# Kernel optimization log

Hardware: AMD Instinct MI355X
Metric: run time of the kernel (lower is better)

The kernel has to match this reference:

```python
import jax, jax.numpy as jnp
import numpy as np

B, T, D, H, HS = 2, 256, 2048, 32, 64
LORA, DLORA, ST = 32, 64, 66  # maa lora rank, decay lora rank, state rows (2+HS)
EPS = 1e-5


def setup_inputs() -> dict:
    key = jax.random.key(0)
    ks = jax.random.split(key, 24)
    n = lambda k, sh, s=0.02: (jax.random.normal(k, sh, jnp.float32) * s)
    u = lambda k, sh: jax.random.uniform(k, sh, jnp.float32)
    return {
        "x": jax.random.normal(ks[0], (B, T, D), jnp.float32),
        "state": jax.random.normal(ks[1], (B, ST, D), jnp.float32) * 0.1,
        "ln1_w": jnp.ones((D,), jnp.float32),
        "ln1_b": jnp.zeros((D,), jnp.float32),
        "time_maa_x": u(ks[2], (D,)),
        "time_maa_w1": n(ks[3], (D, 5 * LORA)),
        "time_maa_w2": n(ks[4], (5, LORA, D)),
        "time_maa_k": u(ks[5], (D,)),
        "time_maa_w": u(ks[6], (D,)),
        "time_maa_v": u(ks[7], (D,)),
        "time_maa_r": u(ks[8], (D,)),
        "time_maa_g": u(ks[9], (D,)),
        "time_decay": n(ks[10], (D,), 0.5),
        "time_decay_w1": n(ks[11], (D, DLORA)),
        "time_decay_w2": n(ks[12], (DLORA, D)),
        "time_faaaa": n(ks[13], (H, HS, 1), 0.1),
        "receptance_weight": n(ks[14], (D, D)),
        "key_weight": n(ks[15], (D, D)),
        "value_weight": n(ks[16], (D, D)),
        "output_weight": n(ks[17], (D, D)),
        "gate_weight": n(ks[18], (D, D)),
        "lnx_w": jnp.ones((D,), jnp.float32),
        "lnx_b": jnp.zeros((D,), jnp.float32),
        "i": 0,
    }


def reference(x, state, ln1_w, ln1_b, time_maa_x, time_maa_w1, time_maa_w2,
              time_maa_k, time_maa_w, time_maa_v, time_maa_r, time_maa_g,
              time_decay, time_decay_w1, time_decay_w2, time_faaaa,
              receptance_weight, key_weight, value_weight, output_weight,
              gate_weight, lnx_w, lnx_b, i):
    # forward() early-returns time_mixing(ln1(x), state, i)
    mu = x.mean(-1, keepdims=True)
    var = ((x - mu) ** 2).mean(-1, keepdims=True)
    x = (x - mu) * jax.lax.rsqrt(var + EPS) * ln1_w + ln1_b

    i1 = (2 + HS) * i + 1
    # token shift: sx[t] = x[t-1] - x[t], with state row i1 as x[-1]
    sx = jnp.concatenate([state[:, i1][:, None] - x[:, :1], x[:, :-1] - x[:, 1:]], axis=1)

    xxx = x + sx * time_maa_x
    t5 = jnp.tanh(xxx @ time_maa_w1).reshape(B, T, 5, LORA)
    xxx5 = jnp.einsum('btfr,frd->btfd', t5, time_maa_w2)          # [B,T,5,D]
    maa = jnp.stack([time_maa_k, time_maa_w, time_maa_v, time_maa_r, time_maa_g])  # [5,D]
    x5 = x[:, :, None] + sx[:, :, None] * (maa + xxx5)            # [B,T,5,D]

    k = (x5[:, :, 0] @ key_weight.T).reshape(B, T, H, HS)
    w = jnp.exp(-jnp.exp(time_decay + jnp.tanh(x5[:, :, 1] @ time_decay_w1) @ time_decay_w2)).reshape(B, T, H, HS)
    v = (x5[:, :, 2] @ value_weight.T).reshape(B, T, H, HS)
    r = (x5[:, :, 3] @ receptance_weight.T).reshape(B, T, H, HS)
    g = jax.nn.silu(x5[:, :, 4] @ gate_weight.T)                  # [B,T,D]

    kv = jnp.einsum('bthi,bthj->bthij', k, v)                     # [B,T,H,HS,HS]
    prev0 = state[:, i1 + 1:i1 + 1 + HS].reshape(B, H, HS, HS)

    def step(prev, xs):
        kv_t, w_t = xs
        return kv_t + w_t[..., None] * prev, prev  # emit state BEFORE update

    _, state_s = jax.lax.scan(step, prev0,
                              (kv.transpose(1, 0, 2, 3, 4), w.transpose(1, 0, 2, 3)))
    state_s = state_s.transpose(1, 0, 2, 3, 4)                    # [B,T,H,HS,HS]

    wkv = time_faaaa * kv + state_s
    rwkv = jnp.einsum('bthj,bthjd->bthd', r, wkv)                 # [B,T,H,HS]

    # GroupNorm(num_groups=H) over each head's HS channels
    gm = rwkv.mean(-1, keepdims=True)
    gv = ((rwkv - gm) ** 2).mean(-1, keepdims=True)
    normed = (rwkv - gm) * jax.lax.rsqrt(gv + EPS)
    normed = normed * lnx_w.reshape(H, HS) + lnx_b.reshape(H, HS)
    normed = normed.reshape(B, T, D)

    return (normed * g) @ output_weight.T
```

## Files before the change

### kernel.cpp

```cpp
#include <hip/hip_runtime.h>
#include <hip/hip_bf16.h>

typedef unsigned short u16;
typedef __attribute__((ext_vector_type(4))) float f32x4;
typedef __attribute__((ext_vector_type(8))) short short8;
typedef __attribute__((ext_vector_type(4))) short bf16x4;

#define B_ 2
#define T_ 256
#define D_ 2048
#define H_ 32
#define HS_ 64
#define M_ 512
#define ST_ 66
#define EPS_ 1e-5f
#define NC_ 16
#define CL_ 16

__device__ __forceinline__ float bf2f(u16 u) {
    union { unsigned int i; float f; } c; c.i = ((unsigned int)u) << 16; return c.f;
}
__device__ __forceinline__ u16 f2bf(float f) {
    union { unsigned int i; float f; } c; c.f = f;
    unsigned int r = c.i + 0x7fffu + ((c.i >> 16) & 1u);
    return (u16)(r >> 16);
}

__device__ __forceinline__ void gld16(const u16* g, u16* l) {
    __builtin_amdgcn_global_load_lds((const __attribute__((address_space(1))) void*)g,
                                     (__attribute__((address_space(3))) void*)l, 16, 0, 0);
}

__global__ __launch_bounds__(256) void wcvt_kernel(const float* __restrict__ wk, const float* __restrict__ wv,
                                                   const float* __restrict__ wr, const float* __restrict__ wg,
                                                   const float* __restrict__ wo, u16* __restrict__ out)
{
    const int wsel = blockIdx.y;
    const float* in = (wsel == 0) ? wk : (wsel == 1) ? wv : (wsel == 2) ? wr : (wsel == 3) ? wg : wo;
    const size_t e = ((size_t)blockIdx.x * 256 + threadIdx.x) * 8;
    f32x4 a = *(const f32x4*)(in + e);
    f32x4 b = *(const f32x4*)(in + e + 4);
    short8 o;
#pragma unroll
    for (int i = 0; i < 4; i++) { o[i] = (short)f2bf(a[i]); o[i + 4] = (short)f2bf(b[i]); }
    *(short8*)(out + (size_t)wsel * D_ * D_ + e) = o;
}

__global__ __launch_bounds__(256) void ln_kernel(const float* __restrict__ x, const float* __restrict__ w,
                                                 const float* __restrict__ bias, float* __restrict__ xln)
{
    const int row = blockIdx.x;
    const float* xr = x + (size_t)row * D_;
    float* orow = xln + (size_t)row * D_;
    const int t = threadIdx.x;
    f32x4 a0 = *(const f32x4*)(xr + t * 8);
    f32x4 a1 = *(const f32x4*)(xr + t * 8 + 4);
    float s = 0.f, q = 0.f;
#pragma unroll
    for (int i = 0; i < 4; i++) { s += a0[i] + a1[i]; q += a0[i]*a0[i] + a1[i]*a1[i]; }
#pragma unroll
    for (int off = 1; off < 64; off <<= 1) { s += __shfl_xor(s, off, 64); q += __shfl_xor(q, off, 64); }
    __shared__ float ls[4], lq[4];
    const int wid = t >> 6, lane = t & 63;
    if (lane == 0) { ls[wid] = s; lq[wid] = q; }
    __syncthreads();
    s = ls[0] + ls[1] + ls[2] + ls[3];
    q = lq[0] + lq[1] + lq[2] + lq[3];
    const float mu = s * (1.f / D_);
    const float var = q * (1.f / D_) - mu * mu;
    const float rs = rsqrtf(var + EPS_);
#pragma unroll
    for (int i = 0; i < 8; i++) {
        int d = t * 8 + i;
        float f = (i < 4) ? a0[i] : a1[i - 4];
        orow[d] = (f - mu) * rs * w[d] + bias[d];
    }
}

__global__ __launch_bounds__(256) void shift_kernel(const float* __restrict__ xln, const float* __restrict__ state,
                                                    const float* __restrict__ maax, const int* __restrict__ ip,
                                                    float* __restrict__ sx, u16* __restrict__ xxxb)
{
    const size_t gid = (size_t)blockIdx.x * 256 + threadIdx.x;
    const size_t e = gid * 4;
    const int row = (int)(e >> 11);
    const int d = (int)(e & 2047);
    const int tt = row & (T_ - 1);
    const int b = row >> 8;
    const float* prev;
    if (tt == 0) prev = state + ((size_t)b * ST_ + (size_t)(66 * ip[0] + 1)) * D_ + d;
    else         prev = xln + e - D_;
    f32x4 p = *(const f32x4*)prev;
    f32x4 c = *(const f32x4*)(xln + e);
    f32x4 mx = *(const f32x4*)(maax + d);
    f32x4 sv;
    bf16x4 xv;
#pragma unroll
    for (int i = 0; i < 4; i++) { sv[i] = p[i] - c[i]; xv[i] = (short)f2bf(c[i] + sv[i] * mx[i]); }
    *(f32x4*)(sx + e) = sv;
    *(bf16x4*)(xxxb + e) = xv;
}

__global__ __launch_bounds__(256) void txp_kernel(const float* __restrict__ in, u16* __restrict__ out,
                                                  int K, int N)
{
    __shared__ float tile[32][33];
    const int k0 = blockIdx.x * 32, n0 = blockIdx.y * 32;
    const int c = threadIdx.x & 31, r8 = threadIdx.x >> 5;
#pragma unroll
    for (int i = 0; i < 4; i++) {
        int r = r8 + i * 8;
        tile[r][c] = in[(size_t)(k0 + r) * N + (n0 + c)];
    }
    __syncthreads();
#pragma unroll
    for (int i = 0; i < 4; i++) {
        int r = r8 + i * 8;
        out[(size_t)(n0 + r) * K + (k0 + c)] = f2bf(tile[c][r]);
    }
}

template<bool TANH>
__global__ __launch_bounds__(512) void wdot_kernel(const u16* __restrict__ A, const u16* __restrict__ Wt,
                                                   float* __restrict__ C, int N)
{
    const int gw = (int)((blockIdx.x * 512 + threadIdx.x) >> 6);
    const int lane = threadIdx.x & 63;
    const int m = gw / N, n = gw - m * N;
    const u16* a = A + (size_t)m * D_ + lane * 8;
    const u16* w = Wt + (size_t)n * D_ + lane * 8;
    float acc = 0.f;
#pragma unroll
    for (int i = 0; i < 4; i++) {
        short8 av = *(const short8*)(a + i * 512);
        short8 wv = *(const short8*)(w + i * 512);
#pragma unroll
        for (int j = 0; j < 8; j++)
            acc = fmaf(bf2f((u16)av[j]), bf2f((u16)wv[j]), acc);
    }
#pragma unroll
    for (int off = 1; off < 64; off <<= 1) acc += __shfl_xor(acc, off, 64);
    if (lane == 0) C[gw] = TANH ? tanhf(acc) : acc;
}

__global__ __launch_bounds__(256) void maa2_kernel(const float* __restrict__ t5, const float* __restrict__ w2,
                                                   const float* __restrict__ xln, const float* __restrict__ sxp,
                                                   const float* __restrict__ mk, const float* __restrict__ mw,
                                                   const float* __restrict__ mv, const float* __restrict__ mr,
                                                   const float* __restrict__ mg, u16* __restrict__ x5)
{
    const int gid = blockIdx.x * 256 + threadIdx.x;
    const int d = gid & (D_ - 1);
    const int f = (gid >> 11) % 5;
    const int mg4 = gid / (5 * D_);
    const float* maa = (f == 0) ? mk : (f == 1) ? mw : (f == 2) ? mv : (f == 3) ? mr : mg;
    const float mf = maa[d];
    const float* w2f = w2 + (size_t)f * 32 * D_ + d;
    const float* t5b = t5 + (size_t)mg4 * 4 * 160 + f * 32;
    float a0 = 0, a1 = 0, a2 = 0, a3 = 0;
#pragma unroll 8
    for (int r = 0; r < 32; r++) {
        float wv = w2f[(size_t)r * D_];
        a0 = fmaf(t5b[r], wv, a0);
        a1 = fmaf(t5b[160 + r], wv, a1);
        a2 = fmaf(t5b[320 + r], wv, a2);
        a3 = fmaf(t5b[480 + r], wv, a3);
    }
    const float accs[4] = {a0, a1, a2, a3};
    const size_t m0 = (size_t)mg4 * 4;
#pragma unroll
    for (int mm = 0; mm < 4; mm++) {
        size_t e = (m0 + mm) * D_ + d;
        x5[(size_t)f * M_ * D_ + e] = f2bf(xln[e] + sxp[e] * (mf + accs[mm]));
    }
}

__global__ __launch_bounds__(256) void decay2_kernel(const float* __restrict__ td, const float* __restrict__ dw2,
                                                     const float* __restrict__ tdec, float* __restrict__ wout)
{
    const int gid = blockIdx.x * 256 + threadIdx.x;
    const int d = gid & (D_ - 1);
    const int mg4 = gid >> 11;
    const float* wp = dw2 + d;
    const float* tb = td + (size_t)mg4 * 4 * 64;
    float a0 = 0, a1 = 0, a2 = 0, a3 = 0;
#pragma unroll 8
    for (int r = 0; r < 64; r++) {
        float wv = wp[(size_t)r * D_];
        a0 = fmaf(tb[r], wv, a0);
        a1 = fmaf(tb[64 + r], wv, a1);
        a2 = fmaf(tb[128 + r], wv, a2);
        a3 = fmaf(tb[192 + r], wv, a3);
    }
    const float base = tdec[d];
    const float accs[4] = {a0, a1, a2, a3};
#pragma unroll
    for (int mm = 0; mm < 4; mm++)
        wout[((size_t)mg4 * 4 + mm) * D_ + d] = expf(-expf(base + accs[mm]));
}

__device__ __forceinline__ void gemm2p_body(const u16* __restrict__ A, const u16* __restrict__ Wb,
                                            float* __restrict__ C, int m0, int n0, int k0, int KC)
{
    __shared__ u16 As[2][128 * 64];
    __shared__ u16 Bs[2][64 * 64];
    const int tid = threadIdx.x;
    const int lane = tid & 63;
    const int wvd = tid >> 6;
    const int wm = (wvd >> 1) * 64;
    const int wn = (wvd & 1) * 32;

    f32x4 acc[4][2];
#pragma unroll
    for (int i = 0; i < 4; i++)
#pragma unroll
        for (int j = 0; j < 2; j++) { acc[i][j][0]=0.f; acc[i][j][1]=0.f; acc[i][j][2]=0.f; acc[i][j][3]=0.f; }

    const int srow = tid >> 3;
    const int sw8  = (((tid & 7) ^ (srow & 7)) << 3);
    const u16* Ag = A + (size_t)(m0 + srow) * D_ + k0 + sw8;
    const u16* Wg = Wb + (size_t)(n0 + srow) * D_ + k0 + sw8;
    const int ldst = tid * 8;

    const int rsw = (lane & 7) << 3;
    const int colb = (lane >> 4) * 8;
    const int fr = lane & 15;

#define STAGE_(bb, kt)                                                            \
    {                                                                             \
        _Pragma("unroll")                                                         \
        for (int i = 0; i < 4; i++)                                               \
            gld16(Ag + (size_t)(i * 32) * D_ + (kt), &As[bb][i * 2048 + ldst]);   \
        _Pragma("unroll")                                                         \
        for (int i = 0; i < 2; i++)                                               \
            gld16(Wg + (size_t)(i * 32) * D_ + (kt), &Bs[bb][i * 2048 + ldst]);   \
    }

    STAGE_(0, 0);
    __syncthreads();
    int cur = 0;
    for (int kt = 0; kt < KC; kt += 64) {
        if (kt + 64 < KC) STAGE_(cur ^ 1, kt + 64);
#pragma unroll
        for (int kk = 0; kk < 64; kk += 32) {
            const int c = (kk + colb) ^ rsw;
            short8 av[4], bv[2];
#pragma unroll
            for (int mi = 0; mi < 4; mi++)
                av[mi] = *(const short8*)&As[cur][(wm + mi * 16 + fr) * 64 + c];
#pragma unroll
            for (int ni = 0; ni < 2; ni++)
                bv[ni] = *(const short8*)&Bs[cur][(wn + ni * 16 + fr) * 64 + c];
#pragma unroll
            for (int mi = 0; mi < 4; mi++)
#pragma unroll
                for (int ni = 0; ni < 2; ni++)
                    acc[mi][ni] = __builtin_amdgcn_mfma_f32_16x16x32_bf16(av[mi], bv[ni], acc[mi][ni], 0, 0, 0);
        }
        __syncthreads();
        cur ^= 1;
    }
#undef STAGE_
    const int cr = wm + (lane >> 4) * 4;
    const int cc = wn + fr;
#pragma unroll
    for (int mi = 0; mi < 4; mi++)
#pragma unroll
        for (int ni = 0; ni < 2; ni++)
#pragma unroll
            for (int j = 0; j < 4; j++)
                C[(size_t)(m0 + cr + mi * 16 + j) * D_ + (n0 + cc + ni * 16)] = acc[mi][ni][j];
}

__global__ __launch_bounds__(256) void gemm4g_kernel(const u16* __restrict__ x5, const u16* __restrict__ wcvt,
                                                     float* __restrict__ kvK, float* __restrict__ kvV,
                                                     float* __restrict__ kvR, float* __restrict__ kvG)
{
    const int s = blockIdx.z;
    const u16* A = x5 + (size_t)(s == 0 ? 0 : s + 1) * M_ * D_;
    const u16* W = wcvt + (size_t)s * D_ * D_;
    float* C = (s == 0) ? kvK : (s == 1) ? kvV : (s == 2) ? kvR : kvG;
    gemm2p_body(A, W, C, blockIdx.y * 128, blockIdx.x * 64, 0, D_);
}

__global__ __launch_bounds__(256) void gemm1g_kernel(const u16* __restrict__ y, const u16* __restrict__ wo,
                                                     float* __restrict__ out, float* __restrict__ p0,
                                                     float* __restrict__ p1, float* __restrict__ p2)
{
    const int ks = blockIdx.z;
    float* C = (ks == 0) ? out : (ks == 1) ? p0 : (ks == 2) ? p1 : p2;
    gemm2p_body(y, wo, C, blockIdx.y * 128, blockIdx.x * 64, ks * 512, 512);
}

__global__ __launch_bounds__(256) void add3_kernel(float* __restrict__ dst, const float* __restrict__ s0,
                                                   const float* __restrict__ s1, const float* __restrict__ s2)
{
    const size_t e = ((size_t)blockIdx.x * 256 + threadIdx.x) * 4;
    f32x4 d = *(const f32x4*)(dst + e);
    f32x4 a = *(const f32x4*)(s0 + e);
    f32x4 b = *(const f32x4*)(s1 + e);
    f32x4 c = *(const f32x4*)(s2 + e);
#pragma unroll
    for (int i = 0; i < 4; i++) d[i] += (a[i] + b[i]) + c[i];
    *(f32x4*)(dst + e) = d;
}

__global__ __launch_bounds__(512) void rec1_kernel(const float* __restrict__ rB, const float* __restrict__ kB,
                                                   const float* __restrict__ wB, const float* __restrict__ vB,
                                                   const float* __restrict__ fa, float* __restrict__ rwkv,
                                                   float* __restrict__ CS, float* __restrict__ RP,
                                                   float* __restrict__ PC)
{
    const int bx = blockIdx.x;
    const int c  = bx & (NC_ - 1);
    const int bh = bx >> 4;
    const int h = bh & 31, b = bh >> 5;
    const int tid = threadIdx.x;
    const int wv = tid >> 6, lane = tid & 63;
    const int wg = wv >> 2;
    const int jb = lane >> 3, dsub = lane & 7;
    const int jbase = jb * 8;
    const int d0 = wg * 32 + (wv & 3) * 8 + dsub;

    __shared__ float stage[4][CL_][64];
    __shared__ float p2[CL_][8][64];
    __shared__ float p1[CL_][8];
    __shared__ float rpS[CL_ * 64];

    float S[8], pv[8], faj[8];
#pragma unroll
    for (int q = 0; q < 8; q++) { S[q] = 0.f; pv[q] = 1.f; faj[q] = fa[h * 64 + jbase + q]; }

    const size_t base = ((size_t)b * T_ * H_ + h) * HS_;
    const int t0 = c * CL_;
    const int arr = wv & 3;
    const float* mysrc = (arr == 0) ? rB : (arr == 1) ? kB : (arr == 2) ? wB : vB;
    const int ts0 = wg * 8 + (lane >> 4);
    const int sch = (lane & 15) * 4;
    const bool p1w = (wv == 0 && dsub == 0);

#pragma unroll
    for (int p = 0; p < 2; p++) {
        f32x4 v = *(const f32x4*)(mysrc + base + (size_t)(t0 + ts0 + p * 4) * (H_ * HS_) + sch);
        *(f32x4*)&stage[arr][ts0 + p * 4][sch] = v;
    }
    __syncthreads();

    f32x4 r0 = *(const f32x4*)&stage[0][0][jbase];
    f32x4 r1 = *(const f32x4*)&stage[0][0][jbase + 4];
    f32x4 k0 = *(const f32x4*)&stage[1][0][jbase];
    f32x4 k1 = *(const f32x4*)&stage[1][0][jbase + 4];
    f32x4 w0 = *(const f32x4*)&stage[2][0][jbase];
    f32x4 w1 = *(const f32x4*)&stage[2][0][jbase + 4];
    float vd = stage[3][0][d0];
#pragma unroll
    for (int ts = 0; ts < CL_; ++ts) {
        f32x4 nr0 = r0, nr1 = r1, nk0 = k0, nk1 = k1, nw0 = w0, nw1 = w1;
        float nvd = vd;
        if (ts + 1 < CL_) {
            nr0 = *(const f32x4*)&stage[0][ts + 1][jbase];
            nr1 = *(const f32x4*)&stage[0][ts + 1][jbase + 4];
            nk0 = *(const f32x4*)&stage[1][ts + 1][jbase];
            nk1 = *(const f32x4*)&stage[1][ts + 1][jbase + 4];
            nw0 = *(const f32x4*)&stage[2][ts + 1][jbase];
            nw1 = *(const f32x4*)&stage[2][ts + 1][jbase + 4];
            nvd = stage[3][ts + 1][d0];
        }
        float s1 = 0.f, s2 = 0.f;
#pragma unroll
        for (int q = 0; q < 4; q++) {
            s1 = fmaf(r0[q] * faj[q],     k0[q], s1);
            s1 = fmaf(r1[q] * faj[q + 4], k1[q], s1);
            s2 = fmaf(r0[q], S[q],     s2);
            s2 = fmaf(r1[q], S[q + 4], s2);
        }
        p2[ts][jb][d0 ^ (jb << 3)] = s2;
        if (p1w) {
            p1[ts][jb] = s1;
#pragma unroll
            for (int q = 0; q < 4; q++) {
                rpS[ts * 64 + jbase + q]     = r0[q] * pv[q];
                rpS[ts * 64 + jbase + 4 + q] = r1[q] * pv[q + 4];
            }
        }
#pragma unroll
        for (int q = 0; q < 4; q++) {
            pv[q]     *= w0[q];
            pv[q + 4] *= w1[q];
            S[q]       = fmaf(w0[q], S[q],     k0[q] * vd);
            S[q + 4]   = fmaf(w1[q], S[q + 4], k1[q] * vd);
        }
        r0 = nr0; r1 = nr1; k0 = nk0; k1 = nk1; w0 = nw0; w1 = nw1; vd = nvd;
    }
    __syncthreads();
#pragma unroll
    for (int p = 0; p < 2; p++) {
        const int ts = wv * 2 + p;
        f32x4 p1a = *(const f32x4*)&p1[ts][0];
        f32x4 p1b = *(const f32x4*)&p1[ts][4];
        float s1t = ((p1a[0] + p1a[1]) + (p1a[2] + p1a[3])) +
                    ((p1b[0] + p1b[1]) + (p1b[2] + p1b[3]));
        float s2t = 0.f;
#pragma unroll
        for (int j = 0; j < 8; j++) s2t += p2[ts][j][lane ^ (j << 3)];
        const float vvv = stage[3][ts][lane];
        rwkv[base + (size_t)(t0 + ts) * (H_ * HS_) + lane] = fmaf(vvv, s1t, s2t);
    }
    RP[(size_t)bx * (CL_ * 64) + tid]       = rpS[tid];
    RP[(size_t)bx * (CL_ * 64) + 512 + tid] = rpS[512 + tid];
#pragma unroll
    for (int q = 0; q < 8; q++)
        CS[(size_t)bx * 4096 + (size_t)(jbase + q) * 64 + d0] = S[q];
    if (p1w) {
#pragma unroll
        for (int q = 0; q < 8; q++)
            PC[(size_t)bx * 64 + jbase + q] = pv[q];
    }
}

__global__ __launch_bounds__(512) void rec2_kernel(const float* __restrict__ state, const int* __restrict__ ip,
                                                   float* __restrict__ CS, const float* __restrict__ PC)
{
    const int bh = blockIdx.x;
    const int b = bh >> 5, h = bh & 31;
    const int tid = threadIdx.x;
    const int o = tid * 8;
    const int jrow = tid >> 3;
    const float* Sp = state + (size_t)b * ST_ * D_ + (size_t)(66 * ip[0] + 2) * D_ + (size_t)h * HS_ * HS_;
    f32x4 c0 = *(const f32x4*)(Sp + o);
    f32x4 c1 = *(const f32x4*)(Sp + o + 4);
    for (int c = 0; c < NC_; ++c) {
        float* cs = CS + ((size_t)(bh * NC_ + c)) * 4096 + o;
        f32x4 l0 = *(const f32x4*)cs;
        f32x4 l1 = *(const f32x4*)(cs + 4);
        const float pc = PC[(size_t)(bh * NC_ + c) * 64 + jrow];
        f32x4 n0, n1;
#pragma unroll
        for (int i = 0; i < 4; i++) { n0[i] = fmaf(pc, c0[i], l0[i]); n1[i] = fmaf(pc, c1[i], l1[i]); }
        *(f32x4*)cs = c0;
        *(f32x4*)(cs + 4) = c1;
        c0 = n0; c1 = n1;
    }
}

__global__ __launch_bounds__(256) void rec3_kernel(const float* __restrict__ CS, const float* __restrict__ RP,
                                                   float* __restrict__ rwkv)
{
    const int bx = blockIdx.x;
    const int c  = bx & (NC_ - 1);
    const int bh = bx >> 4;
    const int h = bh & 31, b = bh >> 5;
    const int tid = threadIdx.x;
    __shared__ float Ss[4096];
    __shared__ float rp[CL_ * 64];
#pragma unroll
    for (int i = 0; i < 4; i++)
        *(f32x4*)&Ss[tid * 4 + i * 1024] = *(const f32x4*)(CS + (size_t)bx * 4096 + tid * 4 + i * 1024);
    *(f32x4*)&rp[tid * 4] = *(const f32x4*)(RP + (size_t)bx * (CL_ * 64) + tid * 4);
    __syncthreads();
    const int tl = tid >> 4;
    const int d4 = (tid & 15) * 4;
    f32x4 acc; acc[0] = acc[1] = acc[2] = acc[3] = 0.f;
    const float* rpr = &rp[tl * 64];
#pragma unroll 16
    for (int j = 0; j < 64; ++j) {
        const float rv = rpr[j];
        const f32x4 sv = *(const f32x4*)&Ss[j * 64 + d4];
#pragma unroll
        for (int i = 0; i < 4; i++) acc[i] = fmaf(rv, sv[i], acc[i]);
    }
    const size_t base = ((size_t)b * T_ * H_ + h) * HS_;
    float* o = rwkv + base + (size_t)(c * CL_ + tl) * (H_ * HS_) + d4;
    f32x4 cur = *(const f32x4*)o;
#pragma unroll
    for (int i = 0; i < 4; i++) cur[i] += acc[i];
    *(f32x4*)o = cur;
}

__global__ __launch_bounds__(256) void gn_kernel(const float* __restrict__ rwkv, const float* __restrict__ gpre,
                                                 const float* __restrict__ lnxw, const float* __restrict__ lnxb,
                                                 u16* __restrict__ y)
{
    const int g = blockIdx.x * 4 + (threadIdx.x >> 6);
    const int lane = threadIdx.x & 63;
    const size_t e = (size_t)g * 64 + lane;
    const float val = rwkv[e];
    float s = val, q = val * val;
#pragma unroll
    for (int off = 1; off < 64; off <<= 1) { s += __shfl_xor(s, off, 64); q += __shfl_xor(q, off, 64); }
    const float mu = s * (1.f / 64.f);
    const float var = q * (1.f / 64.f) - mu * mu;
    const float rs = rsqrtf(var + EPS_);
    const int hj = (int)(e & (size_t)(D_ - 1));
    const float nrm = (val - mu) * rs * lnxw[hj] + lnxb[hj];
    const float gp = gpre[e];
    const float gv = gp / (1.f + expf(-gp));
    y[e] = f2bf(nrm * gv);
}

extern "C" void kernel_launch(void* const* d_in, const int* in_sizes, int n_in,
                              void* d_out, int out_size, void* d_ws, size_t ws_size,
                              hipStream_t stream)
{
    const float* x     = (const float*)d_in[0];
    const float* state = (const float*)d_in[1];
    const float* ln1w  = (const float*)d_in[2];
    const float* ln1b  = (const float*)d_in[3];
    const float* maax  = (const float*)d_in[4];
    const float* w1    = (const float*)d_in[5];
    const float* w2    = (const float*)d_in[6];
    const float* maak  = (const float*)d_in[7];
    const float* maaw  = (const float*)d_in[8];
    const float* maav  = (const float*)d_in[9];
    const float* maar  = (const float*)d_in[10];
    const float* maag  = (const float*)d_in[11];
    const float* tdec  = (const float*)d_in[12];
    const float* dw1   = (const float*)d_in[13];
    const float* dw2   = (const float*)d_in[14];
    const float* fa    = (const float*)d_in[15];
    const float* wrec  = (const float*)d_in[16];
    const float* wkey  = (const float*)d_in[17];
    const float* wval  = (const float*)d_in[18];
    const float* wout  = (const float*)d_in[19];
    const float* wgate = (const float*)d_in[20];
    const float* lnxw  = (const float*)d_in[21];
    const float* lnxb  = (const float*)d_in[22];
    const int*   ip    = (const int*)d_in[23];

    char* ws = (char*)d_ws;
    const size_t MD = (size_t)M_ * D_;
    u16*   wcvt = (u16*)  (ws);
    float* xln  = (float*)(ws + ((size_t)40 << 20));
    float* sx   = (float*)(ws + ((size_t)44 << 20));
    u16*   xxxb = (u16*)  (ws + ((size_t)48 << 20));
    u16*   w1t  = (u16*)  (ws + ((size_t)50 << 20));
    u16*   dw1t = (u16*)  (ws + ((size_t)51 << 20));
    float* t5   = (float*)(ws + ((size_t)52 << 20));
    float* td   = (float*)(ws + ((size_t)53 << 20));
    u16*   x5   = (u16*)  (ws + ((size_t)54 << 20));
    float* wdec = (float*)(ws + ((size_t)64 << 20));
    float* kvK  = (float*)(ws + ((size_t)40 << 20));
    float* kvV  = (float*)(ws + ((size_t)44 << 20));
    float* kvR  = (float*)(ws + ((size_t)48 << 20));
    float* kvG  = (float*)(ws + ((size_t)68 << 20));
    float* rwkv = (float*)(ws + ((size_t)72 << 20));
    u16*   y    = (u16*)  (ws + ((size_t)76 << 20));
    float* CS   = (float*)(ws);
    float* RP   = (float*)(ws + ((size_t)16 << 20));
    float* PC   = (float*)(ws + ((size_t)20 << 20));
    float* pp0  = (float*)(ws + ((size_t)54 << 20));
    float* pp1  = (float*)(ws + ((size_t)58 << 20));
    float* pp2  = (float*)(ws + ((size_t)62 << 20));
    float* out  = (float*)d_out;

    hipLaunchKernelGGL(wcvt_kernel,   dim3(2048, 5),  dim3(256), 0, stream, wkey, wval, wrec, wgate, wout, wcvt);
    hipLaunchKernelGGL(ln_kernel,     dim3(512),      dim3(256), 0, stream, x, ln1w, ln1b, xln);
    hipLaunchKernelGGL(shift_kernel,  dim3(1024),     dim3(256), 0, stream, xln, state, maax, ip, sx, xxxb);
    hipLaunchKernelGGL(txp_kernel,    dim3(64, 5),    dim3(256), 0, stream, w1, w1t, D_, 160);
    hipLaunchKernelGGL(txp_kernel,    dim3(64, 2),    dim3(256), 0, stream, dw1, dw1t, D_, 64);
    hipLaunchKernelGGL((wdot_kernel<true>), dim3(10240), dim3(512), 0, stream, xxxb, w1t, t5, 160);
    hipLaunchKernelGGL(maa2_kernel,   dim3(5120),     dim3(256), 0, stream, t5, w2, xln, sx, maak, maaw, maav, maar, maag, x5);
    hipLaunchKernelGGL((wdot_kernel<true>), dim3(4096), dim3(512), 0, stream, x5 + MD, dw1t, td, 64);
    hipLaunchKernelGGL(decay2_kernel, dim3(1024),     dim3(256), 0, stream, td, dw2, tdec, wdec);
    hipLaunchKernelGGL(gemm4g_kernel, dim3(32, 4, 4), dim3(256), 0, stream, x5, wcvt, kvK, kvV, kvR, kvG);
    hipLaunchKernelGGL(rec1_kernel,   dim3(B_ * H_ * NC_), dim3(512), 0, stream, kvR, kvK, wdec, kvV, fa, rwkv, CS, RP, PC);
    hipLaunchKernelGGL(rec2_kernel,   dim3(B_ * H_),  dim3(512), 0, stream, state, ip, CS, PC);
    hipLaunchKernelGGL(rec3_kernel,   dim3(B_ * H_ * NC_), dim3(256), 0, stream, CS, RP, rwkv);
    hipLaunchKernelGGL(gn_kernel,     dim3(4096),     dim3(256), 0, stream, rwkv, kvG, lnxw, lnxb, y);
    hipLaunchKernelGGL(gemm1g_kernel, dim3(32, 4, 4), dim3(256), 0, stream, y, wcvt + (size_t)4 * D_ * D_, out, pp0, pp1, pp2);
    hipLaunchKernelGGL(add3_kernel,   dim3(1024),     dim3(256), 0, stream, out, pp0, pp1, pp2);

    (void)in_sizes; (void)n_in; (void)out_size; (void)ws_size;
}
```

Baseline: 197.4 us.

## Fuse weight bf16 conversion into GEMM loads, merge rec3 with groupnorm, restructure maa2

Removes the separate weight-conversion pass. The GEMMs now read fp32 weights straight from global memory, convert them to bf16 in registers and write them into swizzled LDS. This removes a full read and write of five 2048x2048 matrices, but doubles the bytes each GEMM block loads for B and drops async global_load_lds for that operand. The rec3 and groupnorm kernels are fused so rwkv is not written and read back. maa2 now handles all five mixes per thread, reusing the xln and sx loads across them.

```diff
diff --git a/kernel.cpp b/kernel.cpp
--- a/kernel.cpp
+++ b/kernel.cpp
@@ -25,25 +25,14 @@
     unsigned int r = c.i + 0x7fffu + ((c.i >> 16) & 1u);
     return (u16)(r >> 16);
 }
+__device__ __forceinline__ u16 f2bf_hw(float f) {
+    __hip_bfloat16 b = __float2bfloat16(f);
+    return *reinterpret_cast<u16*>(&b);
+}
 
 __device__ __forceinline__ void gld16(const u16* g, u16* l) {
     __builtin_amdgcn_global_load_lds((const __attribute__((address_space(1))) void*)g,
                                      (__attribute__((address_space(3))) void*)l, 16, 0, 0);
-}
-
-__global__ __launch_bounds__(256) void wcvt_kernel(const float* __restrict__ wk, const float* __restrict__ wv,
-                                                   const float* __restrict__ wr, const float* __restrict__ wg,
-                                                   const float* __restrict__ wo, u16* __restrict__ out)
-{
-    const int wsel = blockIdx.y;
-    const float* in = (wsel == 0) ? wk : (wsel == 1) ? wv : (wsel == 2) ? wr : (wsel == 3) ? wg : wo;
-    const size_t e = ((size_t)blockIdx.x * 256 + threadIdx.x) * 8;
-    f32x4 a = *(const f32x4*)(in + e);
-    f32x4 b = *(const f32x4*)(in + e + 4);
-    short8 o;
-#pragma unroll
-    for (int i = 0; i < 4; i++) { o[i] = (short)f2bf(a[i]); o[i + 4] = (short)f2bf(b[i]); }
-    *(short8*)(out + (size_t)wsel * D_ * D_ + e) = o;
 }
 
 __global__ __launch_bounds__(256) void ln_kernel(const float* __restrict__ x, const float* __restrict__ w,
@@ -151,27 +140,36 @@
 {
     const int gid = blockIdx.x * 256 + threadIdx.x;
     const int d = gid & (D_ - 1);
-    const int f = (gid >> 11) % 5;
-    const int mg4 = gid / (5 * D_);
-    const float* maa = (f == 0) ? mk : (f == 1) ? mw : (f == 2) ? mv : (f == 3) ? mr : mg;
-    const float mf = maa[d];
-    const float* w2f = w2 + (size_t)f * 32 * D_ + d;
-    const float* t5b = t5 + (size_t)mg4 * 4 * 160 + f * 32;
-    float a0 = 0, a1 = 0, a2 = 0, a3 = 0;
+    const int mg4 = gid >> 11;
+    const size_t m0 = (size_t)mg4 * 4;
+    float xl[4], sv[4];
+#pragma unroll
+    for (int mm = 0; mm < 4; mm++) {
+        const size_t e = (m0 + mm) * D_ + d;
+        xl[mm] = xln[e];
+        sv[mm] = sxp[e];
+    }
+    const float* t5b = t5 + m0 * 160;
+#pragma unroll
+    for (int f = 0; f < 5; f++) {
+        const float* maa = (f == 0) ? mk : (f == 1) ? mw : (f == 2) ? mv : (f == 3) ? mr : mg;
+        const float mf = maa[d];
+        const float* w2f = w2 + (size_t)f * 32 * D_ + d;
+        float a0 = 0, a1 = 0, a2 = 0, a3 = 0;
 #pragma unroll 8
-    for (int r = 0; r < 32; r++) {
-        float wv = w2f[(size_t)r * D_];
-        a0 = fmaf(t5b[r], wv, a0);
-        a1 = fmaf(t5b[160 + r], wv, a1);
-        a2 = fmaf(t5b[320 + r], wv, a2);
-        a3 = fmaf(t5b[480 + r], wv, a3);
-    }
-    const float accs[4] = {a0, a1, a2, a3};
-    const size_t m0 = (size_t)mg4 * 4;
-#pragma unroll
-    for (int mm = 0; mm < 4; mm++) {
-        size_t e = (m0 + mm) * D_ + d;
-        x5[(size_t)f * M_ * D_ + e] = f2bf(xln[e] + sxp[e] * (mf + accs[mm]));
+        for (int r = 0; r < 32; r++) {
+            const float wv = w2f[(size_t)r * D_];
+            a0 = fmaf(t5b[f * 32 + r], wv, a0);
+            a1 = fmaf(t5b[160 + f * 32 + r], wv, a1);
+            a2 = fmaf(t5b[320 + f * 32 + r], wv, a2);
+            a3 = fmaf(t5b[480 + f * 32 + r], wv, a3);
+        }
+        const float accs[4] = {a0, a1, a2, a3};
+#pragma unroll
+        for (int mm = 0; mm < 4; mm++) {
+            const size_t e = (m0 + mm) * D_ + d;
+            x5[(size_t)f * M_ * D_ + e] = f2bf(xl[mm] + sv[mm] * (mf + accs[mm]));
+        }
     }
 }
 
@@ -199,7 +197,7 @@
         wout[((size_t)mg4 * 4 + mm) * D_ + d] = expf(-expf(base + accs[mm]));
 }
 
-__device__ __forceinline__ void gemm2p_body(const u16* __restrict__ A, const u16* __restrict__ Wb,
+__device__ __forceinline__ void gemm2p_body(const u16* __restrict__ A, const float* __restrict__ Wf,
                                             float* __restrict__ C, int m0, int n0, int k0, int KC)
 {
     __shared__ u16 As[2][128 * 64];
@@ -219,28 +217,48 @@
     const int srow = tid >> 3;
     const int sw8  = (((tid & 7) ^ (srow & 7)) << 3);
     const u16* Ag = A + (size_t)(m0 + srow) * D_ + k0 + sw8;
-    const u16* Wg = Wb + (size_t)(n0 + srow) * D_ + k0 + sw8;
     const int ldst = tid * 8;
+
+    const int br  = tid >> 2;
+    const int bc0 = (tid & 3) * 16;
+    const float* Wg = Wf + (size_t)(n0 + br) * D_ + k0 + bc0;
+    const int bb0 = bc0 >> 3;
+    const int dst0 = br * 64 + ((bb0 ^ (br & 7)) << 3);
+    const int dst1 = br * 64 + (((bb0 + 1) ^ (br & 7)) << 3);
 
     const int rsw = (lane & 7) << 3;
     const int colb = (lane >> 4) * 8;
     const int fr = lane & 15;
 
-#define STAGE_(bb, kt)                                                            \
+    f32x4 bl0, bl1, bl2, bl3;
+#define LOADB_(kt) { bl0 = *(const f32x4*)(Wg + (kt));      bl1 = *(const f32x4*)(Wg + (kt) + 4);  \
+                     bl2 = *(const f32x4*)(Wg + (kt) + 8);  bl3 = *(const f32x4*)(Wg + (kt) + 12); }
+#define STAGEA_(bb, kt)                                                           \
     {                                                                             \
         _Pragma("unroll")                                                         \
         for (int i = 0; i < 4; i++)                                               \
             gld16(Ag + (size_t)(i * 32) * D_ + (kt), &As[bb][i * 2048 + ldst]);   \
+    }
+#define WRITEB_(bb)                                                               \
+    {                                                                             \
+        short8 p0, p1;                                                            \
         _Pragma("unroll")                                                         \
-        for (int i = 0; i < 2; i++)                                               \
-            gld16(Wg + (size_t)(i * 32) * D_ + (kt), &Bs[bb][i * 2048 + ldst]);   \
-    }
-
-    STAGE_(0, 0);
+        for (int j = 0; j < 4; j++) {                                             \
+            p0[j]     = (short)f2bf_hw(bl0[j]); p0[j + 4] = (short)f2bf_hw(bl1[j]); \
+            p1[j]     = (short)f2bf_hw(bl2[j]); p1[j + 4] = (short)f2bf_hw(bl3[j]); \
+        }                                                                         \
+        *(short8*)&Bs[bb][dst0] = p0;                                             \
+        *(short8*)&Bs[bb][dst1] = p1;                                             \
+    }
+
+    LOADB_(0);
+    STAGEA_(0, 0);
+    WRITEB_(0);
     __syncthreads();
     int cur = 0;
     for (int kt = 0; kt < KC; kt += 64) {
-        if (kt + 64 < KC) STAGE_(cur ^ 1, kt + 64);
+        const bool more = kt + 64 < KC;
+        if (more) { LOADB_(kt + 64); STAGEA_(cur ^ 1, kt + 64); }
 #pragma unroll
         for (int kk = 0; kk < 64; kk += 32) {
             const int c = (kk + colb) ^ rsw;
@@ -257,10 +275,13 @@
                 for (int ni = 0; ni < 2; ni++)
                     acc[mi][ni] = __builtin_amdgcn_mfma_f32_16x16x32_bf16(av[mi], bv[ni], acc[mi][ni], 0, 0, 0);
         }
+        if (more) WRITEB_(cur ^ 1);
         __syncthreads();
         cur ^= 1;
     }
-#undef STAGE_
+#undef LOADB_
+#undef STAGEA_
+#undef WRITEB_
     const int cr = wm + (lane >> 4) * 4;
     const int cc = wn + fr;
 #pragma unroll
@@ -272,18 +293,20 @@
                 C[(size_t)(m0 + cr + mi * 16 + j) * D_ + (n0 + cc + ni * 16)] = acc[mi][ni][j];
 }
 
-__global__ __launch_bounds__(256) void gemm4g_kernel(const u16* __restrict__ x5, const u16* __restrict__ wcvt,
-                                                     float* __restrict__ kvK, float* __restrict__ kvV,
-                                                     float* __restrict__ kvR, float* __restrict__ kvG)
+__global__ __launch_bounds__(256) void gemm4g_kernel(const u16* __restrict__ x5, const float* __restrict__ Wk,
+                                                     const float* __restrict__ Wv, const float* __restrict__ Wr,
+                                                     const float* __restrict__ Wg, float* __restrict__ kvK,
+                                                     float* __restrict__ kvV, float* __restrict__ kvR,
+                                                     float* __restrict__ kvG)
 {
     const int s = blockIdx.z;
     const u16* A = x5 + (size_t)(s == 0 ? 0 : s + 1) * M_ * D_;
-    const u16* W = wcvt + (size_t)s * D_ * D_;
+    const float* W = (s == 0) ? Wk : (s == 1) ? Wv : (s == 2) ? Wr : Wg;
     float* C = (s == 0) ? kvK : (s == 1) ? kvV : (s == 2) ? kvR : kvG;
     gemm2p_body(A, W, C, blockIdx.y * 128, blockIdx.x * 64, 0, D_);
 }
 
-__global__ __launch_bounds__(256) void gemm1g_kernel(const u16* __restrict__ y, const u16* __restrict__ wo,
+__global__ __launch_bounds__(256) void gemm1g_kernel(const u16* __restrict__ y, const float* __restrict__ wo,
                                                      float* __restrict__ out, float* __restrict__ p0,
                                                      float* __restrict__ p1, float* __restrict__ p2)
 {
@@ -443,8 +466,10 @@
     }
 }
 
-__global__ __launch_bounds__(256) void rec3_kernel(const float* __restrict__ CS, const float* __restrict__ RP,
-                                                   float* __restrict__ rwkv)
+__global__ __launch_bounds__(256) void rec3gn_kernel(const float* __restrict__ CS, const float* __restrict__ RP,
+                                                     const float* __restrict__ rwkv, const float* __restrict__ gpre,
+                                                     const float* __restrict__ lnxw, const float* __restrict__ lnxb,
+                                                     u16* __restrict__ y)
 {
     const int bx = blockIdx.x;
     const int c  = bx & (NC_ - 1);
@@ -470,32 +495,29 @@
         for (int i = 0; i < 4; i++) acc[i] = fmaf(rv, sv[i], acc[i]);
     }
     const size_t base = ((size_t)b * T_ * H_ + h) * HS_;
-    float* o = rwkv + base + (size_t)(c * CL_ + tl) * (H_ * HS_) + d4;
-    f32x4 cur = *(const f32x4*)o;
-#pragma unroll
-    for (int i = 0; i < 4; i++) cur[i] += acc[i];
-    *(f32x4*)o = cur;
-}
-
-__global__ __launch_bounds__(256) void gn_kernel(const float* __restrict__ rwkv, const float* __restrict__ gpre,
-                                                 const float* __restrict__ lnxw, const float* __restrict__ lnxb,
-                                                 u16* __restrict__ y)
-{
-    const int g = blockIdx.x * 4 + (threadIdx.x >> 6);
-    const int lane = threadIdx.x & 63;
-    const size_t e = (size_t)g * 64 + lane;
-    const float val = rwkv[e];
-    float s = val, q = val * val;
-#pragma unroll
-    for (int off = 1; off < 64; off <<= 1) { s += __shfl_xor(s, off, 64); q += __shfl_xor(q, off, 64); }
+    const size_t eb = base + (size_t)(c * CL_ + tl) * (H_ * HS_);
+    const f32x4 cur = *(const f32x4*)(rwkv + eb + d4);
+    f32x4 val;
+#pragma unroll
+    for (int i = 0; i < 4; i++) val[i] = cur[i] + acc[i];
+    float s = 0.f, q = 0.f;
+#pragma unroll
+    for (int i = 0; i < 4; i++) { s += val[i]; q += val[i] * val[i]; }
+#pragma unroll
+    for (int off = 1; off < 16; off <<= 1) { s += __shfl_xor(s, off, 64); q += __shfl_xor(q, off, 64); }
     const float mu = s * (1.f / 64.f);
     const float var = q * (1.f / 64.f) - mu * mu;
     const float rs = rsqrtf(var + EPS_);
-    const int hj = (int)(e & (size_t)(D_ - 1));
-    const float nrm = (val - mu) * rs * lnxw[hj] + lnxb[hj];
-    const float gp = gpre[e];
-    const float gv = gp / (1.f + expf(-gp));
-    y[e] = f2bf(nrm * gv);
+    bf16x4 yv;
+#pragma unroll
+    for (int i = 0; i < 4; i++) {
+        const int hj = h * 64 + d4 + i;
+        const float nrm = (val[i] - mu) * rs * lnxw[hj] + lnxb[hj];
+        const float gp = gpre[eb + d4 + i];
+        const float gv = gp / (1.f + expf(-gp));
+        yv[i] = (short)f2bf(nrm * gv);
+    }
+    *(bf16x4*)(y + eb + d4) = yv;
 }
 
 extern "C" void kernel_launch(void* const* d_in, const int* in_sizes, int n_in,
@@ -529,7 +551,9 @@
 
     char* ws = (char*)d_ws;
     const size_t MD = (size_t)M_ * D_;
-    u16*   wcvt = (u16*)  (ws);
+    float* CS   = (float*)(ws);
+    float* RP   = (float*)(ws + ((size_t)16 << 20));
+    float* PC   = (float*)(ws + ((size_t)20 << 20));
     float* xln  = (float*)(ws + ((size_t)40 << 20));
     float* sx   = (float*)(ws + ((size_t)44 << 20));
     u16*   xxxb = (u16*)  (ws + ((size_t)48 << 20));
@@ -545,29 +569,24 @@
     float* kvG  = (float*)(ws + ((size_t)68 << 20));
     float* rwkv = (float*)(ws + ((size_t)72 << 20));
     u16*   y    = (u16*)  (ws + ((size_t)76 << 20));
-    float* CS   = (float*)(ws);
-    float* RP   = (float*)(ws + ((size_t)16 << 20));
-    float* PC   = (float*)(ws + ((size_t)20 << 20));
     float* pp0  = (float*)(ws + ((size_t)54 << 20));
     float* pp1  = (float*)(ws + ((size_t)58 << 20));
     float* pp2  = (float*)(ws + ((size_t)62 << 20));
     float* out  = (float*)d_out;
 
-    hipLaunchKernelGGL(wcvt_kernel,   dim3(2048, 5),  dim3(256), 0, stream, wkey, wval, wrec, wgate, wout, wcvt);
     hipLaunchKernelGGL(ln_kernel,     dim3(512),      dim3(256), 0, stream, x, ln1w, ln1b, xln);
     hipLaunchKernelGGL(shift_kernel,  dim3(1024),     dim3(256), 0, stream, xln, state, maax, ip, sx, xxxb);
     hipLaunchKernelGGL(txp_kernel,    dim3(64, 5),    dim3(256), 0, stream, w1, w1t, D_, 160);
     hipLaunchKernelGGL(txp_kernel,    dim3(64, 2),    dim3(256), 0, stream, dw1, dw1t, D_, 64);
     hipLaunchKernelGGL((wdot_kernel<true>), dim3(10240), dim3(512), 0, stream, xxxb, w1t, t5, 160);
-    hipLaunchKernelGGL(maa2_kernel,   dim3(5120),     dim3(256), 0, stream, t5, w2, xln, sx, maak, maaw, maav, maar, maag, x5);
+    hipLaunchKernelGGL(maa2_kernel,   dim3(1024),     dim3(256), 0, stream, t5, w2, xln, sx, maak, maaw, maav, maar, maag, x5);
     hipLaunchKernelGGL((wdot_kernel<true>), dim3(4096), dim3(512), 0, stream, x5 + MD, dw1t, td, 64);
     hipLaunchKernelGGL(decay2_kernel, dim3(1024),     dim3(256), 0, stream, td, dw2, tdec, wdec);
-    hipLaunchKernelGGL(gemm4g_kernel, dim3(32, 4, 4), dim3(256), 0, stream, x5, wcvt, kvK, kvV, kvR, kvG);
+    hipLaunchKernelGGL(gemm4g_kernel, dim3(32, 4, 4), dim3(256), 0, stream, x5, wkey, wval, wrec, wgate, kvK, kvV, kvR, kvG);
     hipLaunchKernelGGL(rec1_kernel,   dim3(B_ * H_ * NC_), dim3(512), 0, stream, kvR, kvK, wdec, kvV, fa, rwkv, CS, RP, PC);
     hipLaunchKernelGGL(rec2_kernel,   dim3(B_ * H_),  dim3(512), 0, stream, state, ip, CS, PC);
-    hipLaunchKernelGGL(rec3_kernel,   dim3(B_ * H_ * NC_), dim3(256), 0, stream, CS, RP, rwkv);
-    hipLaunchKernelGGL(gn_kernel,     dim3(4096),     dim3(256), 0, stream, rwkv, kvG, lnxw, lnxb, y);
-    hipLaunchKernelGGL(gemm1g_kernel, dim3(32, 4, 4), dim3(256), 0, stream, y, wcvt + (size_t)4 * D_ * D_, out, pp0, pp1, pp2);
+    hipLaunchKernelGGL(rec3gn_kernel, dim3(B_ * H_ * NC_), dim3(256), 0, stream, CS, RP, rwkv, kvG, lnxw, lnxb, y);
+    hipLaunchKernelGGL(gemm1g_kernel, dim3(32, 4, 4), dim3(256), 0, stream, y, wout, out, pp0, pp1, pp2);
     hipLaunchKernelGGL(add3_kernel,   dim3(1024),     dim3(256), 0, stream, out, pp0, pp1, pp2);
 
     (void)in_sizes; (void)n_in; (void)out_size; (void)ws_size;
```

Measured after the change: 183.7 us. 1.07x faster.
